# Optimization experiments

Hardware: AMD Instinct MI355X
Metric: run time of the kernel (lower is better)

The kernel has to match this reference:

```python
import jax, jax.numpy as jnp
import numpy as np

N = 100000   # nodes
E = 3200000  # edges (avg degree 32)
D = 2        # spatial dim (2D collective motion)
C = 1.0      # spring constant c
R_C = 1.0    # rest length r_c
P = 2        # potential exponent p
GAMMA = 0.1  # damping gamma
EPS = 1e-12  # torch F.normalize eps


def setup_inputs() -> dict:
    key = jax.random.key(0)
    k1, k2, k3, k4 = jax.random.split(key, 4)
    x = jax.random.normal(k1, (N, D), dtype=jnp.float32) * 10.0  # positions
    v = jax.random.normal(k2, (N, D), dtype=jnp.float32)          # velocities
    src = jax.random.randint(k3, (E,), 0, N)                      # edge sources
    dst = jax.random.randint(k4, (E,), 0, N)                      # edge destinations
    return {"x": x, "v": v, "src": src, "dst": dst}


def reference(x, v, src, dst):
    # calc_message: dr = dst_pos - src_pos (non-periodic euclid distance)
    dr = x[dst] - x[src]                                   # [E, D]
    abs_dr = jnp.linalg.norm(dr, axis=-1, keepdims=True)   # [E, 1]
    unit_dr = dr / jnp.maximum(abs_dr, EPS)                # F.normalize
    force = -C * P * (abs_dr - R_C) ** (P - 1)             # spring force magnitude
    m = force * unit_dr                                    # [E, D] message
    # update_all: fn.sum of messages at dst nodes -> acceleration
    a = jax.ops.segment_sum(m, dst, num_segments=N)        # [N, D]
    # damping term
    return a - GAMMA * v
```

## Files before the change

### kernel.cpp

```cpp
#include <hip/hip_runtime.h>

#define GAMMA 0.1f
#define EPS_F 1e-12f

#define S_NODES 200
#define PMAX 512
#define BK 256
#define BK_THREADS 1024

__global__ __launch_bounds__(BK_THREADS)
void count_kernel(const int4* __restrict__ dst4, const int* __restrict__ dst,
                  int* __restrict__ cnts, int e, int P, int chunk) {
    __shared__ int hist[PMAX];
    int tid = threadIdx.x, b = blockIdx.x;
    for (int i = tid; i < PMAX; i += BK_THREADS) hist[i] = 0;
    __syncthreads();
    int e4 = e >> 2;
    long gs = (long)b * chunk;
    long ge = gs + chunk; if (ge > e4) ge = e4;
    for (long i = gs + tid; i < ge; i += BK_THREADS) {
        int4 d4 = dst4[i];
        atomicAdd(&hist[d4.x / S_NODES], 1);
        atomicAdd(&hist[d4.y / S_NODES], 1);
        atomicAdd(&hist[d4.z / S_NODES], 1);
        atomicAdd(&hist[d4.w / S_NODES], 1);
    }
    if (b == BK - 1) {
        for (int i = e4 * 4 + tid; i < e; i += BK_THREADS)
            atomicAdd(&hist[dst[i] / S_NODES], 1);
    }
    __syncthreads();
    for (int k = tid; k < PMAX; k += BK_THREADS)
        cnts[(long)b * PMAX + k] = hist[k];
}

__global__ __launch_bounds__(PMAX)
void offset_kernel(int* __restrict__ cnts, int* __restrict__ starts,
                   int e, int P) {
    __shared__ int sc[PMAX];
    int k = threadIdx.x;
    int total = 0;
    if (k < P)
        for (int b = 0; b < BK; ++b) total += cnts[(long)b * PMAX + k];
    sc[k] = total;
    __syncthreads();
    for (int off = 1; off < PMAX; off <<= 1) {
        int vv = (k >= off) ? sc[k - off] : 0;
        __syncthreads();
        sc[k] += vv;
        __syncthreads();
    }
    int start = sc[k] - total;
    if (k < P) {
        starts[k] = start;
        if (k == P - 1) starts[P] = start + total;
        int run = start;
        for (int b = 0; b < BK; ++b) {
            int c = cnts[(long)b * PMAX + k];
            cnts[(long)b * PMAX + k] = run;
            run += c;
        }
    }
}

__device__ __forceinline__ void scatter_one(int s, int d, int* loff,
                                            int* __restrict__ buckets) {
    int p = d / S_NODES;
    int r = atomicAdd(&loff[p], 1);
    buckets[r] = (s << 8) | (d - p * S_NODES);
}

__global__ __launch_bounds__(BK_THREADS)
void scatter_kernel(const int4* __restrict__ src4, const int4* __restrict__ dst4,
                    const int* __restrict__ src, const int* __restrict__ dst,
                    const int* __restrict__ cnts, int* __restrict__ buckets,
                    int e, int P, int chunk) {
    __shared__ int loff[PMAX];
    int tid = threadIdx.x, b = blockIdx.x;
    for (int i = tid; i < PMAX; i += BK_THREADS)
        loff[i] = cnts[(long)b * PMAX + i];
    __syncthreads();
    int e4 = e >> 2;
    long gs = (long)b * chunk;
    long ge = gs + chunk; if (ge > e4) ge = e4;
    for (long i = gs + tid; i < ge; i += BK_THREADS) {
        int4 s4 = src4[i];
        int4 d4 = dst4[i];
        scatter_one(s4.x, d4.x, loff, buckets);
        scatter_one(s4.y, d4.y, loff, buckets);
        scatter_one(s4.z, d4.z, loff, buckets);
        scatter_one(s4.w, d4.w, loff, buckets);
    }
    if (b == BK - 1) {
        for (int i = e4 * 4 + tid; i < e; i += BK_THREADS)
            scatter_one(src[i], dst[i], loff, buckets);
    }
}

__global__ __launch_bounds__(1024)
void scan_kernel(const float2* __restrict__ x, const float2* __restrict__ v,
                 const int* __restrict__ buckets, const int* __restrict__ starts,
                 float2* __restrict__ out, int n) {
    __shared__ float2 acc[S_NODES];
    int k = blockIdx.x, tid = threadIdx.x;
    int lo = k * S_NODES;
    for (int i = tid; i < S_NODES; i += 1024) acc[i] = make_float2(0.f, 0.f);
    __syncthreads();
    int s0 = starts[k], s1 = starts[k + 1];
    for (int i = s0 + tid; i < s1; i += 1024) {
        int w = buckets[i];
        int s = w >> 8;
        int dl = w & 255;
        float2 xs = x[s];
        float2 xd = x[lo + dl];
        float dx = xd.x - xs.x;
        float dy = xd.y - xs.y;
        float r = sqrtf(dx * dx + dy * dy);
        float sc = -2.0f * (r - 1.0f) / fmaxf(r, EPS_F);
        atomicAdd(&acc[dl].x, sc * dx);
        atomicAdd(&acc[dl].y, sc * dy);
    }
    __syncthreads();
    for (int i = tid; i < S_NODES; i += 1024) {
        int g = lo + i;
        if (g < n) {
            float2 vi = v[g];
            out[g] = make_float2(acc[i].x - GAMMA * vi.x,
                                 acc[i].y - GAMMA * vi.y);
        }
    }
}

__global__ void init_out_kernel(const float2* __restrict__ v,
                                float2* __restrict__ out, int n) {
    int i = blockIdx.x * blockDim.x + threadIdx.x;
    if (i < n) {
        float2 vi = v[i];
        out[i] = make_float2(-GAMMA * vi.x, -GAMMA * vi.y);
    }
}

__device__ __forceinline__ void do_edge_atomic(const float2* __restrict__ x,
                                               int s, int d,
                                               float* __restrict__ out) {
    float2 xs = x[s];
    float2 xd = x[d];
    float dx = xd.x - xs.x;
    float dy = xd.y - xs.y;
    float r = sqrtf(dx * dx + dy * dy);
    float sc = -2.0f * (r - 1.0f) / fmaxf(r, EPS_F);
    atomicAdd(&out[2 * d], sc * dx);
    atomicAdd(&out[2 * d + 1], sc * dy);
}

__global__ void edge_kernel_atomic(const float2* __restrict__ x,
                                   const int4* __restrict__ src4,
                                   const int4* __restrict__ dst4,
                                   const int* __restrict__ src,
                                   const int* __restrict__ dst,
                                   float* __restrict__ out,
                                   int e4, int e_total) {
    int i = blockIdx.x * blockDim.x + threadIdx.x;
    if (i < e4) {
        int4 s = src4[i];
        int4 d = dst4[i];
        do_edge_atomic(x, s.x, d.x, out);
        do_edge_atomic(x, s.y, d.y, out);
        do_edge_atomic(x, s.z, d.z, out);
        do_edge_atomic(x, s.w, d.w, out);
    }
    if (i == 0) {
        for (int ee = e4 * 4; ee < e_total; ++ee)
            do_edge_atomic(x, src[ee], dst[ee], out);
    }
}

extern "C" void kernel_launch(void* const* d_in, const int* in_sizes, int n_in,
                              void* d_out, int out_size, void* d_ws, size_t ws_size,
                              hipStream_t stream) {
    const float2* x = (const float2*)d_in[0];
    const float2* v = (const float2*)d_in[1];
    const int* src  = (const int*)d_in[2];
    const int* dst  = (const int*)d_in[3];

    int n = in_sizes[0] / 2;
    int e = in_sizes[2];

    float2* out = (float2*)d_out;

    int P = (n + S_NODES - 1) / S_NODES;

    size_t off_starts = (size_t)BK * PMAX * sizeof(int);
    size_t off_buckets = (off_starts + (PMAX + 1) * sizeof(int) + 255) & ~(size_t)255;
    size_t need = off_buckets + (size_t)e * sizeof(int);

    if (P <= PMAX && n < (1 << 24) && ws_size >= need) {
        int* cnts = (int*)d_ws;
        int* starts = (int*)((char*)d_ws + off_starts);
        int* buckets = (int*)((char*)d_ws + off_buckets);

        int e4 = e >> 2;
        int chunk = (e4 + BK - 1) / BK;

        count_kernel<<<BK, BK_THREADS, 0, stream>>>(
            (const int4*)dst, dst, cnts, e, P, chunk);
        offset_kernel<<<1, PMAX, 0, stream>>>(cnts, starts, e, P);
        scatter_kernel<<<BK, BK_THREADS, 0, stream>>>(
            (const int4*)src, (const int4*)dst, src, dst,
            cnts, buckets, e, P, chunk);
        scan_kernel<<<P, 1024, 0, stream>>>(
            x, v, buckets, starts, out, n);
    } else {
        int threads = 256;
        init_out_kernel<<<(n + threads - 1) / threads, threads, 0, stream>>>(
            v, out, n);
        int e4 = e / 4;
        int blocks = (e4 + threads - 1) / threads;
        if (blocks < 1) blocks = 1;
        edge_kernel_atomic<<<blocks, threads, 0, stream>>>(
            x, (const int4*)src, (const int4*)dst, src, dst, (float*)out, e4, e);
    }
}
```

Measured before the change: 152.6 us.

## Parallelize per-bucket offset scan with transposed counts and wave-level column scans

The count matrix is stored transposed (bucket-major), so each bucket's per-block counts are contiguous. A new multi-block kernel scans each column with one 64-lane wavefront using int4 loads and shuffles, writing relative offsets and per-bucket totals. A small single-block kernel then prefix-sums the totals, and the scatter kernel adds the bucket start to each relative offset. This replaces a single-block kernel in which each thread walked 256 strided entries twice, at the cost of one extra kernel launch.

```diff
diff --git a/kernel.cpp b/kernel.cpp
--- a/kernel.cpp
+++ b/kernel.cpp
@@ -10,7 +10,7 @@
 
 __global__ __launch_bounds__(BK_THREADS)
 void count_kernel(const int4* __restrict__ dst4, const int* __restrict__ dst,
-                  int* __restrict__ cnts, int e, int P, int chunk) {
+                  int* __restrict__ cnts, int e, int chunk) {
     __shared__ int hist[PMAX];
     int tid = threadIdx.x, b = blockIdx.x;
     for (int i = tid; i < PMAX; i += BK_THREADS) hist[i] = 0;
@@ -31,18 +31,39 @@
     }
     __syncthreads();
     for (int k = tid; k < PMAX; k += BK_THREADS)
-        cnts[(long)b * PMAX + k] = hist[k];
+        cnts[(long)k * BK + b] = hist[k];
+}
+
+__global__ __launch_bounds__(1024)
+void colscan_kernel(int* __restrict__ cnts, int* __restrict__ totals) {
+    int wid = (blockIdx.x * blockDim.x + threadIdx.x) >> 6;
+    int lane = threadIdx.x & 63;
+    if (wid >= PMAX) return;
+    int4* col = (int4*)(cnts + (long)wid * BK);
+    int4 vv = col[lane];
+    int lt = vv.x + vv.y + vv.z + vv.w;
+    int inc = lt;
+    #pragma unroll
+    for (int off = 1; off < 64; off <<= 1) {
+        int t = __shfl_up(inc, off);
+        if (lane >= off) inc += t;
+    }
+    int ex = inc - lt;
+    int4 bb;
+    bb.x = ex;
+    bb.y = ex + vv.x;
+    bb.z = ex + vv.x + vv.y;
+    bb.w = ex + vv.x + vv.y + vv.z;
+    col[lane] = bb;
+    if (lane == 63) totals[wid] = inc;
 }
 
 __global__ __launch_bounds__(PMAX)
-void offset_kernel(int* __restrict__ cnts, int* __restrict__ starts,
-                   int e, int P) {
+void prefix_kernel(const int* __restrict__ totals, int* __restrict__ starts) {
     __shared__ int sc[PMAX];
     int k = threadIdx.x;
-    int total = 0;
-    if (k < P)
-        for (int b = 0; b < BK; ++b) total += cnts[(long)b * PMAX + k];
-    sc[k] = total;
+    int t = totals[k];
+    sc[k] = t;
     __syncthreads();
     for (int off = 1; off < PMAX; off <<= 1) {
         int vv = (k >= off) ? sc[k - off] : 0;
@@ -50,17 +71,8 @@
         sc[k] += vv;
         __syncthreads();
     }
-    int start = sc[k] - total;
-    if (k < P) {
-        starts[k] = start;
-        if (k == P - 1) starts[P] = start + total;
-        int run = start;
-        for (int b = 0; b < BK; ++b) {
-            int c = cnts[(long)b * PMAX + k];
-            cnts[(long)b * PMAX + k] = run;
-            run += c;
-        }
-    }
+    starts[k] = sc[k] - t;
+    if (k == PMAX - 1) starts[PMAX] = sc[k];
 }
 
 __device__ __forceinline__ void scatter_one(int s, int d, int* loff,
@@ -73,12 +85,12 @@
 __global__ __launch_bounds__(BK_THREADS)
 void scatter_kernel(const int4* __restrict__ src4, const int4* __restrict__ dst4,
                     const int* __restrict__ src, const int* __restrict__ dst,
-                    const int* __restrict__ cnts, int* __restrict__ buckets,
-                    int e, int P, int chunk) {
+                    const int* __restrict__ cnts, const int* __restrict__ starts,
+                    int* __restrict__ buckets, int e, int chunk) {
     __shared__ int loff[PMAX];
     int tid = threadIdx.x, b = blockIdx.x;
     for (int i = tid; i < PMAX; i += BK_THREADS)
-        loff[i] = cnts[(long)b * PMAX + i];
+        loff[i] = cnts[(long)i * BK + b] + starts[i];
     __syncthreads();
     int e4 = e >> 2;
     long gs = (long)b * chunk;
@@ -190,12 +202,14 @@
 
     int P = (n + S_NODES - 1) / S_NODES;
 
-    size_t off_starts = (size_t)BK * PMAX * sizeof(int);
+    size_t off_totals = (size_t)PMAX * BK * sizeof(int);
+    size_t off_starts = off_totals + PMAX * sizeof(int);
     size_t off_buckets = (off_starts + (PMAX + 1) * sizeof(int) + 255) & ~(size_t)255;
     size_t need = off_buckets + (size_t)e * sizeof(int);
 
     if (P <= PMAX && n < (1 << 24) && ws_size >= need) {
         int* cnts = (int*)d_ws;
+        int* totals = (int*)((char*)d_ws + off_totals);
         int* starts = (int*)((char*)d_ws + off_starts);
         int* buckets = (int*)((char*)d_ws + off_buckets);
 
@@ -203,11 +217,12 @@
         int chunk = (e4 + BK - 1) / BK;
 
         count_kernel<<<BK, BK_THREADS, 0, stream>>>(
-            (const int4*)dst, dst, cnts, e, P, chunk);
-        offset_kernel<<<1, PMAX, 0, stream>>>(cnts, starts, e, P);
+            (const int4*)dst, dst, cnts, e, chunk);
+        colscan_kernel<<<(PMAX * 64) / 1024, 1024, 0, stream>>>(cnts, totals);
+        prefix_kernel<<<1, PMAX, 0, stream>>>(totals, starts);
         scatter_kernel<<<BK, BK_THREADS, 0, stream>>>(
             (const int4*)src, (const int4*)dst, src, dst,
-            cnts, buckets, e, P, chunk);
+            cnts, starts, buckets, e, chunk);
         scan_kernel<<<P, 1024, 0, stream>>>(
             x, v, buckets, starts, out, n);
     } else {
```

Result: faster. 138.9 us (-9.0%).
